# Kernel tuning notes

Measured on AMD Instinct MI355X. Metric: run time of the kernel, lower is better.

The kernel has to match this reference:

```python
import jax, jax.numpy as jnp
import numpy as np

B, G, K, A = 2, 50000, 32, 64  # batch, grid points, neighbors, ao_vals


def setup_inputs() -> dict:
    key = jax.random.key(0)
    k1, k2, k3, k4 = jax.random.split(key, 4)
    out = jax.random.normal(k1, (B, G, A), dtype=jnp.float32)
    # neighbor indices in [0, G]; index G points at the zero padding row
    coords_neighbors_idx = jax.random.randint(k2, (G, K), 0, G + 1, dtype=jnp.int32)
    scale = 1.0 / np.sqrt(A)
    W2 = jax.random.normal(k3, (A, A), dtype=jnp.float32) * scale
    b2 = jnp.zeros((A,), dtype=jnp.float32)
    W3 = jax.random.normal(k4, (A, A), dtype=jnp.float32) * scale
    b3 = jnp.zeros((A,), dtype=jnp.float32)
    return {"out": out, "coords_neighbors_idx": coords_neighbors_idx,
            "W2": W2, "b2": b2, "W3": W3, "b3": b3}


def reference(out, coords_neighbors_idx, W2, b2, W3, b3):
    n_batch, n_grid, n_ao = out.shape
    # pad grid axis with a zero row so index n_grid gathers zeros
    pad = jnp.concatenate([out, jnp.zeros((n_batch, 1, n_ao), out.dtype)], axis=1)
    # gather neighbors: [B, G, K, A], then sum-aggregate over neighbors
    messages = jnp.take(pad, coords_neighbors_idx, axis=1).sum(axis=2)  # [B, G, A]
    messages = messages @ W2 + b2  # dense_2 (activation=None)
    y = out + messages             # residual
    y = y @ W3 + b3                # dense_3 (activation=None)
    return y
```

## Files before the change

kernel.cpp:

```cpp
#include <hip/hip_runtime.h>
#include <hip/hip_fp16.h>


constexpr int A   = 64;
constexpr int K   = 32;
constexpr int GPB = 32;
constexpr int XS  = 136;

typedef _Float16 f16x8 __attribute__((ext_vector_type(8)));
typedef float    f32x4 __attribute__((ext_vector_type(4)));

__global__ void prep_kernel(const float* __restrict__ W2, const float* __restrict__ b2,
                            const float* __restrict__ W3, const float* __restrict__ b3,
                            __half* __restrict__ WTg, float* __restrict__ bb,
                            const float2* __restrict__ out2,
                            __half2* __restrict__ packed,
                            const int* __restrict__ nbr, int* __restrict__ nbrs,
                            const int G, const int packB) {
  const int tid = threadIdx.x;
  if (blockIdx.x < 16) {
    const int e = blockIdx.x * 256 + tid;
    const int n = e >> 6, k = e & 63;
    float acc = 0.f;
#pragma unroll
    for (int q = 0; q < A; ++q) acc = fmaf(W2[k * A + q], W3[q * A + n], acc);
    WTg[n * 128 + k]     = __float2half(acc);
    WTg[n * 128 + A + k] = __float2half(W3[k * A + n]);
    if (blockIdx.x == 0 && tid < A) {
      float b = b3[tid];
#pragma unroll
      for (int q = 0; q < A; ++q) b = fmaf(b2[q], W3[q * A + tid], b);
      bb[tid] = b;
    }
    return;
  }
  if (blockIdx.x < 16 + packB) {
    const int d = (blockIdx.x - 16) * 256 + tid;
    const int total = (G + 1) * 64;
    if (d >= total) return;
    const int g = d >> 6, c = d & 63;
    float2 v = make_float2(0.f, 0.f);
    if (g < G) {
      const int b = c >> 5;
      v = out2[(size_t)b * (G * 32) + (size_t)g * 32 + (c & 31)];
    }
    packed[d] = __floats2half2_rn(v.x, v.y);
    return;
  }
  const int r = (blockIdx.x - 16 - packB) * 8 + (tid >> 5);
  const int slot = tid & 31;
  if (r >= G) return;
  int v = nbr[(size_t)r * K + slot];
#pragma unroll
  for (int k = 2; k <= 32; k <<= 1) {
#pragma unroll
    for (int j = k >> 1; j >= 1; j >>= 1) {
      const int o = __shfl_xor(v, j);
      const bool dir = ((slot & k) == 0);
      const bool takeMin = (((slot & j) == 0) == dir);
      v = takeMin ? min(v, o) : max(v, o);
    }
  }
  nbrs[(size_t)r * K + slot] = v;
}

__global__ __launch_bounds__(256, 8) void fused_kernel(
    const __half2* __restrict__ packed, const int* __restrict__ nbrs,
    const __half* __restrict__ WTg, const float* __restrict__ bb,
    float* __restrict__ y, const int G) {
  __shared__ __half X[64 * XS];

  const int tid = threadIdx.x;
  const int lane = tid & 63;
  const int w = __builtin_amdgcn_readfirstlane(tid >> 6);
  const int gbase = blockIdx.x * GPB;
  const int gcount = min(GPB, G - gbase);
  const int e = lane & 31;
  const int rb = (lane >> 5) * 32;

  const __half2 z = __floats2half2_rn(0.f, 0.f);

#pragma unroll
  for (int gg = 0; gg < 8; ++gg) {
    const int gl = w * 8 + gg;
    if (gl < gcount) {
      const int g = gbase + gl;
      const int* np = nbrs + (size_t)g * K;
      __half2 m0 = z, m1 = z, m2 = z, m3 = z;
#pragma unroll
      for (int k = 0; k < K; k += 4) {
        const __half2 u0 = packed[(size_t)np[k]     * 64 + lane];
        const __half2 u1 = packed[(size_t)np[k + 1] * 64 + lane];
        const __half2 u2 = packed[(size_t)np[k + 2] * 64 + lane];
        const __half2 u3 = packed[(size_t)np[k + 3] * 64 + lane];
        m0 = __hadd2(m0, u0);
        m1 = __hadd2(m1, u1);
        m2 = __hadd2(m2, u2);
        m3 = __hadd2(m3, u3);
      }
      const __half2 m = __hadd2(__hadd2(m0, m1), __hadd2(m2, m3));
      const __half2 o = packed[(size_t)g * 64 + lane];
      const int r = rb + gl;
      *(__half2*)&X[r * XS + 2 * e]     = m;
      *(__half2*)&X[r * XS + A + 2 * e] = o;
    }
  }
  __syncthreads();

  const int quad = lane >> 4;
  const int mn = lane & 15;
  f32x4 acc0 = {0.f, 0.f, 0.f, 0.f};
  f32x4 acc1 = {0.f, 0.f, 0.f, 0.f};
  f32x4 acc2 = {0.f, 0.f, 0.f, 0.f};
  f32x4 acc3 = {0.f, 0.f, 0.f, 0.f};
#pragma unroll
  for (int kt = 0; kt < 4; ++kt) {
    const int ko = kt * 32 + quad * 8;
    const f16x8 a = *(const f16x8*)&X[(w * 16 + mn) * XS + ko];
    const f16x8 b0 = *(const f16x8*)&WTg[(0 * 16 + mn) * 128 + ko];
    acc0 = __builtin_amdgcn_mfma_f32_16x16x32_f16(a, b0, acc0, 0, 0, 0);
    const f16x8 b1 = *(const f16x8*)&WTg[(1 * 16 + mn) * 128 + ko];
    acc1 = __builtin_amdgcn_mfma_f32_16x16x32_f16(a, b1, acc1, 0, 0, 0);
    const f16x8 b2 = *(const f16x8*)&WTg[(2 * 16 + mn) * 128 + ko];
    acc2 = __builtin_amdgcn_mfma_f32_16x16x32_f16(a, b2, acc2, 0, 0, 0);
    const f16x8 b3 = *(const f16x8*)&WTg[(3 * 16 + mn) * 128 + ko];
    acc3 = __builtin_amdgcn_mfma_f32_16x16x32_f16(a, b3, acc3, 0, 0, 0);
  }

  f32x4 accs[4] = {acc0, acc1, acc2, acc3};
#pragma unroll
  for (int nt = 0; nt < 4; ++nt) {
    const int col = nt * 16 + mn;
    const float bv = bb[col];
#pragma unroll
    for (int rg = 0; rg < 4; ++rg) {
      const int row = w * 16 + quad * 4 + rg;
      const int b = row >> 5, gl = row & 31;
      if (gl < gcount)
        y[((size_t)b * G + (gbase + gl)) * 64 + col] = accs[nt][rg] + bv;
    }
  }
}

extern "C" void kernel_launch(void* const* d_in, const int* in_sizes, int n_in,
                              void* d_out, int out_size, void* d_ws, size_t ws_size,
                              hipStream_t stream) {
  const float* out = (const float*)d_in[0];
  const int*   nbr = (const int*)d_in[1];
  const float* W2  = (const float*)d_in[2];
  const float* b2  = (const float*)d_in[3];
  const float* W3  = (const float*)d_in[4];
  const float* b3  = (const float*)d_in[5];
  float* y = (float*)d_out;
  const int G = in_sizes[1] / K;

  __half2* packed = (__half2*)d_ws;
  const size_t packedBytes = (size_t)(G + 1) * 64 * sizeof(__half2);
  __half* WTg = (__half*)((char*)d_ws + packedBytes);
  float* bb = (float*)((char*)d_ws + packedBytes + 8192 * sizeof(__half));
  int* nbrs = (int*)((char*)d_ws + packedBytes + 8192 * sizeof(__half)
                     + 64 * sizeof(float));

  const int packTotal = (G + 1) * 64;
  const int packB = (packTotal + 255) / 256;
  const int sortB = (G + 7) / 8;
  prep_kernel<<<16 + packB + sortB, 256, 0, stream>>>(
      W2, b2, W3, b3, WTg, bb, (const float2*)out, packed, nbr, nbrs, G, packB);

  const int blocks = (G + GPB - 1) / GPB;
  fused_kernel<<<blocks, 256, 0, stream>>>(packed, nbrs, WTg, bb, y, G);
}
```

Before: 146.3 us.

## Transpose sorted neighbor indices per block and interleave gathers across grid points

The prep kernel now sorts each block's 32 neighbor rows, then writes them through shared memory in a k-major layout per 32-point block, padding out-of-range rows with the zero-row index. In the fused kernel, each wave keeps 16 half2 accumulators for its 8 grid points and walks the neighbor slots, so 8 independent gathers are in flight per step. The index loads become contiguous per k, and the extra memory-level parallelism is meant to hide gather latency. In exchange it uses more registers, which may reduce occupancy, and adds a shared-memory transpose and a barrier to the prep stage.

```diff
diff --git a/kernel.cpp b/kernel.cpp
--- a/kernel.cpp
+++ b/kernel.cpp
@@ -15,7 +15,7 @@
                             __half* __restrict__ WTg, float* __restrict__ bb,
                             const float2* __restrict__ out2,
                             __half2* __restrict__ packed,
-                            const int* __restrict__ nbr, int* __restrict__ nbrs,
+                            const int* __restrict__ nbr, int* __restrict__ nbrsT,
                             const int G, const int packB) {
   const int tid = threadIdx.x;
   if (blockIdx.x < 16) {
@@ -47,25 +47,42 @@
     packed[d] = __floats2half2_rn(v.x, v.y);
     return;
   }
-  const int r = (blockIdx.x - 16 - packB) * 8 + (tid >> 5);
+  const int fb = blockIdx.x - 16 - packB;
+  __shared__ int S[32 * 33];
+  const int half = tid >> 5;
   const int slot = tid & 31;
-  if (r >= G) return;
-  int v = nbr[(size_t)r * K + slot];
 #pragma unroll
-  for (int k = 2; k <= 32; k <<= 1) {
+  for (int it = 0; it < 4; ++it) {
+    const int gl = it * 8 + half;
+    const int r = fb * GPB + gl;
+    int v;
+    if (r < G) {
+      v = nbr[(size_t)r * K + slot];
 #pragma unroll
-    for (int j = k >> 1; j >= 1; j >>= 1) {
-      const int o = __shfl_xor(v, j);
-      const bool dir = ((slot & k) == 0);
-      const bool takeMin = (((slot & j) == 0) == dir);
-      v = takeMin ? min(v, o) : max(v, o);
+      for (int kk = 2; kk <= 32; kk <<= 1) {
+#pragma unroll
+        for (int j = kk >> 1; j >= 1; j >>= 1) {
+          const int o = __shfl_xor(v, j);
+          const bool dir = ((slot & kk) == 0);
+          const bool takeMin = (((slot & j) == 0) == dir);
+          v = takeMin ? min(v, o) : max(v, o);
+        }
+      }
+    } else {
+      v = G;
     }
+    S[slot * 33 + gl] = v;
   }
-  nbrs[(size_t)r * K + slot] = v;
+  __syncthreads();
+#pragma unroll
+  for (int it = 0; it < 4; ++it) {
+    const int d = it * 256 + tid;
+    nbrsT[(size_t)fb * (K * GPB) + d] = S[(d >> 5) * 33 + (d & 31)];
+  }
 }
 
 __global__ __launch_bounds__(256, 8) void fused_kernel(
-    const __half2* __restrict__ packed, const int* __restrict__ nbrs,
+    const __half2* __restrict__ packed, const int* __restrict__ nbrsT,
     const __half* __restrict__ WTg, const float* __restrict__ bb,
     float* __restrict__ y, const int G) {
   __shared__ __half X[64 * XS];
@@ -83,27 +100,33 @@
 #pragma unroll
   for (int gg = 0; gg < 8; ++gg) {
     const int gl = w * 8 + gg;
-    if (gl < gcount) {
-      const int g = gbase + gl;
-      const int* np = nbrs + (size_t)g * K;
-      __half2 m0 = z, m1 = z, m2 = z, m3 = z;
+    const int g = (gl < gcount) ? (gbase + gl) : G;
+    *(__half2*)&X[(rb + gl) * XS + A + 2 * e] = packed[(size_t)g * 64 + lane];
+  }
+
+  const int* base = nbrsT + (size_t)blockIdx.x * (K * GPB) + w * 8;
+  __half2 ma[8], mb[8];
 #pragma unroll
-      for (int k = 0; k < K; k += 4) {
-        const __half2 u0 = packed[(size_t)np[k]     * 64 + lane];
-        const __half2 u1 = packed[(size_t)np[k + 1] * 64 + lane];
-        const __half2 u2 = packed[(size_t)np[k + 2] * 64 + lane];
-        const __half2 u3 = packed[(size_t)np[k + 3] * 64 + lane];
-        m0 = __hadd2(m0, u0);
-        m1 = __hadd2(m1, u1);
-        m2 = __hadd2(m2, u2);
-        m3 = __hadd2(m3, u3);
-      }
-      const __half2 m = __hadd2(__hadd2(m0, m1), __hadd2(m2, m3));
-      const __half2 o = packed[(size_t)g * 64 + lane];
-      const int r = rb + gl;
-      *(__half2*)&X[r * XS + 2 * e]     = m;
-      *(__half2*)&X[r * XS + A + 2 * e] = o;
+  for (int gg = 0; gg < 8; ++gg) { ma[gg] = z; mb[gg] = z; }
+
+#pragma unroll 2
+  for (int k = 0; k < K; k += 2) {
+#pragma unroll
+    for (int gg = 0; gg < 8; ++gg) {
+      const int i0 = base[k * GPB + gg];
+      ma[gg] = __hadd2(ma[gg], packed[(size_t)i0 * 64 + lane]);
     }
+#pragma unroll
+    for (int gg = 0; gg < 8; ++gg) {
+      const int i1 = base[(k + 1) * GPB + gg];
+      mb[gg] = __hadd2(mb[gg], packed[(size_t)i1 * 64 + lane]);
+    }
+  }
+
+#pragma unroll
+  for (int gg = 0; gg < 8; ++gg) {
+    const int gl = w * 8 + gg;
+    *(__half2*)&X[(rb + gl) * XS + 2 * e] = __hadd2(ma[gg], mb[gg]);
   }
   __syncthreads();
 
@@ -154,19 +177,20 @@
   float* y = (float*)d_out;
   const int G = in_sizes[1] / K;
 
+  const int blocks = (G + GPB - 1) / GPB;
+
   __half2* packed = (__half2*)d_ws;
   const size_t packedBytes = (size_t)(G + 1) * 64 * sizeof(__half2);
   __half* WTg = (__half*)((char*)d_ws + packedBytes);
   float* bb = (float*)((char*)d_ws + packedBytes + 8192 * sizeof(__half));
-  int* nbrs = (int*)((char*)d_ws + packedBytes + 8192 * sizeof(__half)
-                     + 64 * sizeof(float));
+  int* nbrsT = (int*)((char*)d_ws + packedBytes + 8192 * sizeof(__half)
+                      + 64 * sizeof(float));
 
   const int packTotal = (G + 1) * 64;
   const int packB = (packTotal + 255) / 256;
-  const int sortB = (G + 7) / 8;
+  const int sortB = blocks;
   prep_kernel<<<16 + packB + sortB, 256, 0, stream>>>(
-      W2, b2, W3, b3, WTg, bb, (const float2*)out, packed, nbr, nbrs, G, packB);
+      W2, b2, W3, b3, WTg, bb, (const float2*)out, packed, nbr, nbrsT, G, packB);
 
-  const int blocks = (G + GPB - 1) / GPB;
-  fused_kernel<<<blocks, 256, 0, stream>>>(packed, nbrs, WTg, bb, y, G);
+  fused_kernel<<<blocks, 256, 0, stream>>>(packed, nbrsT, WTg, bb, y, G);
 }
```

New measurement: 139.1 us. -4.9%, faster.
